# Optimization experiments

Hardware: AMD Instinct MI355X
Metric: run time of the kernel (lower is better)

Reference implementation:

```python
import jax, jax.numpy as jnp
import numpy as np

B, T, D = 256, 512, 32   # batch, seq_len, var_length (== input_size == output_size)
H, L = 256, 2            # hidden_size, num_layers


def setup_inputs() -> dict:
    key = jax.random.key(0)
    ks = jax.random.split(key, 16)
    s = 1.0 / np.sqrt(H)  # PyTorch LSTM/Linear default init range
    def u(k, shape):
        return jax.random.uniform(k, shape, jnp.float32, -s, s)
    inp = {"input": jax.random.normal(ks[0], (B, T, D), jnp.float32)}
    # encoder LSTM (b = b_ih + b_hh folded together); gate order i,f,g,o
    inp["enc_Wih0"] = u(ks[1], (4 * H, D)); inp["enc_Whh0"] = u(ks[2], (4 * H, H)); inp["enc_b0"] = u(ks[3], (4 * H,))
    inp["enc_Wih1"] = u(ks[4], (4 * H, H)); inp["enc_Whh1"] = u(ks[5], (4 * H, H)); inp["enc_b1"] = u(ks[6], (4 * H,))
    # decoder LSTM
    inp["dec_Wih0"] = u(ks[7], (4 * H, D)); inp["dec_Whh0"] = u(ks[8], (4 * H, H)); inp["dec_b0"] = u(ks[9], (4 * H,))
    inp["dec_Wih1"] = u(ks[10], (4 * H, H)); inp["dec_Whh1"] = u(ks[11], (4 * H, H)); inp["dec_b1"] = u(ks[12], (4 * H,))
    # output projection
    inp["fc_W"] = u(ks[13], (D, H)); inp["fc_b"] = u(ks[14], (D,))
    return inp


def _lstm_cell(x, h, c, Wih, Whh, b):
    g = x @ Wih.T + h @ Whh.T + b            # [B, 4H]
    i, f, gg, o = jnp.split(g, 4, axis=-1)   # PyTorch gate order i,f,g,o
    c = jax.nn.sigmoid(f) * c + jax.nn.sigmoid(i) * jnp.tanh(gg)
    h = jax.nn.sigmoid(o) * jnp.tanh(c)
    return h, c


def reference(input, enc_Wih0, enc_Whh0, enc_b0, enc_Wih1, enc_Whh1, enc_b1,
              dec_Wih0, dec_Whh0, dec_b0, dec_Wih1, dec_Whh1, dec_b1, fc_W, fc_b):
    b, t, d = input.shape
    hdim = enc_Whh0.shape[1]
    x = jnp.transpose(input, (1, 0, 2))  # time-major [T, B, D]

    # ----- encoder: 2-layer LSTM, keep final (h, c) per layer -----
    enc = [(enc_Wih0, enc_Whh0, enc_b0), (enc_Wih1, enc_Whh1, enc_b1)]
    hs, cs = [], []
    seq = x
    for Wih, Whh, bb in enc:
        def step(carry, xt, Wih=Wih, Whh=Whh, bb=bb):
            h, c = carry
            h, c = _lstm_cell(xt, h, c, Wih, Whh, bb)
            return (h, c), h
        z = jnp.zeros((b, hdim), input.dtype)
        (hT, cT), seq = jax.lax.scan(step, (z, z), seq)
        hs.append(hT); cs.append(cT)
    h0 = jnp.stack(hs)  # [L, B, H]
    c0 = jnp.stack(cs)

    dec = [(dec_Wih0, dec_Whh0, dec_b0), (dec_Wih1, dec_Whh1, dec_b1)]

    def dec_step(carry, _):
        xt, h, c = carry
        inp_l = xt
        new_h, new_c = [], []
        for l, (Wih, Whh, bb) in enumerate(dec):
            hl, cl = _lstm_cell(inp_l, h[l], c[l], Wih, Whh, bb)
            new_h.append(hl); new_c.append(cl)
            inp_l = hl
        pred = inp_l @ fc_W.T + fc_b  # [B, D]
        return (pred, jnp.stack(new_h), jnp.stack(new_c)), pred

    x0 = jnp.zeros((b, d), input.dtype)
    _, preds = jax.lax.scan(dec_step, (x0, h0, c0), None, length=t)  # [T, B, D]
    # cat along time then reverse (inv_idx)
    out = jnp.transpose(preds, (1, 0, 2))[:, ::-1, :]
    return out
```

## Files before the change

kernel.cpp:

```cpp
#include <hip/hip_runtime.h>

typedef __attribute__((ext_vector_type(8))) short bf16x8;
typedef __attribute__((ext_vector_type(4))) float f32x4;

#define MFMA16(a,b,c) __builtin_amdgcn_mfma_f32_16x16x32_bf16((a),(b),(c),0,0,0)


#define SZ_HBUF   (2*256*256*2)
#define OFF_H0H   0
#define OFF_H0L   (OFF_H0H + SZ_HBUF)
#define OFF_H1H   (OFF_H0L + SZ_HBUF)
#define OFF_H1L   (OFF_H1H + SZ_HBUF)
#define OFF_CFIN  (OFF_H1L + SZ_HBUF)
#define OFF_EW0H  (OFF_CFIN + 524288)
#define OFF_EW0L  (OFF_EW0H + 589824)
#define OFF_EW1H  (OFF_EW0L + 589824)
#define OFF_EW1L  (OFF_EW1H + 1048576)
#define OFF_DW0H  (OFF_EW1L + 1048576)
#define OFF_DW0L  (OFF_DW0H + 1048576)
#define OFF_DW1H  (OFF_DW0L + 1048576)
#define OFF_DW1L  (OFF_DW1H + 1048576)
#define OFF_BEFF  (OFF_DW1L + 1048576)
#define OFF_FCWH  (OFF_BEFF + 4096)
#define OFF_FCWL  (OFF_FCWH + 16384)
#define OFF_EFLG  (OFF_FCWL + 16384)
#define OFF_DFLG  (OFF_EFLG + 4096)

static __device__ __forceinline__ unsigned short f2bf(float f) {
  unsigned u = __float_as_uint(f);
  u = u + 0x7fffu + ((u >> 16) & 1u);
  return (unsigned short)(u >> 16);
}
static __device__ __forceinline__ float bf2f(unsigned short s) {
  return __uint_as_float(((unsigned)s) << 16);
}
static __device__ __forceinline__ float sigf(float x) {
  return 1.f / (1.f + __expf(-x));
}
static __device__ __forceinline__ float tanhsafe(float x) {
  float a = fabsf(x);
  float e = __expf(-2.f * a);
  float t = (1.f - e) / (1.f + e);
  return x < 0.f ? -t : t;
}
static __device__ __forceinline__ void st_hpair(float h, unsigned short* ph, unsigned short* pl) {
  unsigned short hi = f2bf(h);
  unsigned short lo = f2bf(h - bf2f(hi));
  __hip_atomic_store(ph, hi, __ATOMIC_RELAXED, __HIP_MEMORY_SCOPE_AGENT);
  __hip_atomic_store(pl, lo, __ATOMIC_RELAXED, __HIP_MEMORY_SCOPE_AGENT);
}
static __device__ __forceinline__ f32x4 ld16(const void* p) {
  f32x4 d;
  asm volatile("global_load_dwordx4 %0, %1, off sc0 sc1" : "=&v"(d) : "v"(p) : "memory");
  return d;
}
static __device__ __forceinline__ void wait_vm0() {
  asm volatile("s_waitcnt vmcnt(0)" ::: "memory");
  __builtin_amdgcn_sched_barrier(0);
}
static __device__ __forceinline__ void flag_barrier(unsigned* flags, int gc, unsigned round) {
  __syncthreads();
  if (threadIdx.x == 0)
    __hip_atomic_store(flags + gc, round, __ATOMIC_RELAXED, __HIP_MEMORY_SCOPE_AGENT);
  if (threadIdx.x < 64) {
    int l = threadIdx.x;
    for (;;) {
      unsigned v = (l < 16) ? __hip_atomic_load(flags + l, __ATOMIC_RELAXED, __HIP_MEMORY_SCOPE_AGENT)
                            : round;
      if (__all((int)(v >= round))) break;
    }
  }
  __syncthreads();
}

#define LDSF(base, row, kk) \
  (*(const bf16x8*)((base) + ((((row) << 9) | (lrow << 4) | ((kk) << 6)) ^ (((row) & 7) << 4))))

__global__ void k_prep_cat(int nrows, const float* __restrict__ s0, int K0,
                           const float* __restrict__ s1, int K1,
                           unsigned short* __restrict__ whi, unsigned short* __restrict__ wlo) {
  int K = K0 + K1;
  int tot = nrows * K;
  for (int idx = blockIdx.x * blockDim.x + threadIdx.x; idx < tot; idx += gridDim.x * blockDim.x) {
    int n = idx / K, k = idx - n * K;
    float v = (k < K0) ? s0[n * K0 + k] : s1[n * K1 + (k - K0)];
    unsigned short hi = f2bf(v);
    unsigned short lo = f2bf(v - bf2f(hi));
    whi[idx] = hi; wlo[idx] = lo;
  }
}
__global__ void k_prep_dec0(const float* __restrict__ Wih0, const float* __restrict__ Whh0,
                            const float* __restrict__ fcW,
                            unsigned short* __restrict__ whi, unsigned short* __restrict__ wlo) {
  int tot = 1024 * 512;
  for (int idx = blockIdx.x * blockDim.x + threadIdx.x; idx < tot; idx += gridDim.x * blockDim.x) {
    int n = idx >> 9, k = idx & 511;
    float v;
    if (k < 256) {
      v = 0.f;
      #pragma unroll
      for (int d = 0; d < 32; ++d) v += Wih0[n * 32 + d] * fcW[d * 256 + k];
    } else {
      v = Whh0[n * 256 + (k - 256)];
    }
    unsigned short hi = f2bf(v);
    unsigned short lo = f2bf(v - bf2f(hi));
    whi[idx] = hi; wlo[idx] = lo;
  }
}
__global__ void k_prep_beff(const float* __restrict__ Wih0, const float* __restrict__ b0,
                            const float* __restrict__ fcb, float* __restrict__ beff) {
  int n = blockIdx.x * blockDim.x + threadIdx.x;
  if (n < 1024) {
    float v = b0[n];
    #pragma unroll
    for (int d = 0; d < 32; ++d) v += Wih0[n * 32 + d] * fcb[d];
    beff[n] = v;
  }
}

__global__ __launch_bounds__(256, 1)
void k_encoder(const float* __restrict__ input,
               const unsigned short* __restrict__ w0hi, const unsigned short* __restrict__ w0lo,
               const unsigned short* __restrict__ w1hi, const unsigned short* __restrict__ w1lo,
               const float* __restrict__ b0, const float* __restrict__ b1,
               unsigned short* h0h, unsigned short* h0l,
               unsigned short* h1h, unsigned short* h1l,
               float* __restrict__ cfin, unsigned* flags)
{
  const int wg = blockIdx.x;
  const int gb = wg & 15, gc = wg >> 4;
  const int tid = threadIdx.x;
  const int wid = tid >> 6, lane = tid & 63;
  const int lcol = lane & 15, lrow = lane >> 4;
  const int r0 = gb * 16, u0 = gc * 16;
  const int wrow = wid * 256 + u0 + lcol;

  __shared__ char s_h0[2][8192];
  __shared__ char s_h1[2][8192];
  __shared__ float gA[4][16][17];
  __shared__ float gB[4][16][17];
  __shared__ float cb[2][16][16];

  cb[0][tid >> 4][tid & 15] = 0.f;
  cb[1][tid >> 4][tid & 15] = 0.f;

  const int srow = (tid >> 5) & 7;
  const int scol8 = (tid & 31) << 3;
  const int dA = ((srow << 9) | ((tid & 31) << 4)) ^ (srow << 4);
  const int dB = dA + 4096;

  bf16x8 w0h_[9], w0l_[9], w1h_[16], w1l_[16];
  {
    const unsigned short* p = w0hi + (size_t)wrow * 288 + lrow * 8;
    const unsigned short* q = w0lo + (size_t)wrow * 288 + lrow * 8;
    #pragma unroll
    for (int kk = 0; kk < 9; ++kk) {
      w0h_[kk] = *(const bf16x8*)(p + kk * 32);
      w0l_[kk] = *(const bf16x8*)(q + kk * 32);
    }
    const unsigned short* p1 = w1hi + (size_t)wrow * 512 + lrow * 8;
    const unsigned short* q1 = w1lo + (size_t)wrow * 512 + lrow * 8;
    #pragma unroll
    for (int kk = 0; kk < 16; ++kk) {
      w1h_[kk] = *(const bf16x8*)(p1 + kk * 32);
      w1l_[kk] = *(const bf16x8*)(q1 + kk * 32);
    }
  }
  const float bias0 = b0[wrow];
  const float bias1 = b1[wrow];
  unsigned* gflags = flags + gb * 64;
  __syncthreads();

  for (int k = 0; k <= 512; ++k) {
    const int rp = (k - 1) & 1;
    const int wp = k & 1;

    f32x4 ahh = {0.f,0.f,0.f,0.f}, ahl = {0.f,0.f,0.f,0.f}, alh = {0.f,0.f,0.f,0.f};
    union { bf16x8 v; unsigned short s[8]; } xh, xl;
    if (k < 512) {
      const float* px = input + (size_t)(r0 + lcol) * 16384 + (size_t)k * 32 + lrow * 8;
      f32x4 a = *(const f32x4*)px;
      f32x4 b = *(const f32x4*)(px + 4);
      #pragma unroll
      for (int j = 0; j < 4; ++j) {
        unsigned short t1 = f2bf(a[j]); xh.s[j] = t1;     xl.s[j]     = f2bf(a[j] - bf2f(t1));
        unsigned short t2 = f2bf(b[j]); xh.s[4 + j] = t2; xl.s[4 + j] = f2bf(b[j] - bf2f(t2));
      }
    }

    const unsigned short* p0h = h0h + (size_t)rp * 65536 + (size_t)(r0 + srow) * 256 + scol8;
    const unsigned short* p0l = h0l + (size_t)rp * 65536 + (size_t)(r0 + srow) * 256 + scol8;
    const unsigned short* p1h = h1h + (size_t)wp * 65536 + (size_t)(r0 + srow) * 256 + scol8;
    const unsigned short* p1l = h1l + (size_t)wp * 65536 + (size_t)(r0 + srow) * 256 + scol8;
    f32x4 v0 = ld16(p0h), v1 = ld16(p0h + 2048);
    f32x4 v2 = ld16(p0l), v3 = ld16(p0l + 2048);
    f32x4 v4 = ld16(p1h), v5 = ld16(p1h + 2048);
    f32x4 v6 = ld16(p1l), v7 = ld16(p1l + 2048);

    if (k < 512) {
      ahh = MFMA16(xh.v, w0h_[0], ahh);
      ahl = MFMA16(xh.v, w0l_[0], ahl);
      alh = MFMA16(xl.v, w0h_[0], alh);
    }

    wait_vm0();
    *(f32x4*)(s_h0[0] + dA) = v0; *(f32x4*)(s_h0[0] + dB) = v1;
    *(f32x4*)(s_h0[1] + dA) = v2; *(f32x4*)(s_h0[1] + dB) = v3;
    *(f32x4*)(s_h1[0] + dA) = v4; *(f32x4*)(s_h1[0] + dB) = v5;
    *(f32x4*)(s_h1[1] + dA) = v6; *(f32x4*)(s_h1[1] + dB) = v7;
    __syncthreads();

    bf16x8 f0h[8], f0l[8];
    #pragma unroll
    for (int kk = 0; kk < 8; ++kk) {
      f0h[kk] = LDSF(s_h0[0], lcol, kk);
      f0l[kk] = LDSF(s_h0[1], lcol, kk);
    }

    if (k < 512) {
      #pragma unroll
      for (int kk = 0; kk < 8; ++kk) {
        ahh = MFMA16(f0h[kk], w0h_[kk + 1], ahh);
        ahl = MFMA16(f0h[kk], w0l_[kk + 1], ahl);
        alh = MFMA16(f0l[kk], w0h_[kk + 1], alh);
      }
      f32x4 g = ahh + ahl + alh;
      #pragma unroll
      for (int r = 0; r < 4; ++r) gA[wid][lrow * 4 + r][lcol] = g[r] + bias0;
    }
    if (k >= 1) {
      f32x4 bhh = {0.f,0.f,0.f,0.f}, bhl = {0.f,0.f,0.f,0.f}, blh = {0.f,0.f,0.f,0.f};
      #pragma unroll
      for (int kk = 0; kk < 8; ++kk) {
        bhh = MFMA16(f0h[kk], w1h_[kk], bhh);
        bhl = MFMA16(f0h[kk], w1l_[kk], bhl);
        blh = MFMA16(f0l[kk], w1h_[kk], blh);
      }
      #pragma unroll
      for (int kk = 0; kk < 8; ++kk) {
        bf16x8 fh_ = LDSF(s_h1[0], lcol, kk);
        bf16x8 fl_ = LDSF(s_h1[1], lcol, kk);
        bhh = MFMA16(fh_, w1h_[kk + 8], bhh);
        bhl = MFMA16(fh_, w1l_[kk + 8], bhl);
        blh = MFMA16(fl_, w1h_[kk + 8], blh);
      }
      f32x4 g = bhh + bhl + blh;
      #pragma unroll
      for (int r = 0; r < 4; ++r) gB[wid][lrow * 4 + r][lcol] = g[r] + bias1;
    }
    __syncthreads();

    const int urow = tid >> 4, uu = tid & 15;
    if (k < 512) {
      float gi = gA[0][urow][uu], gf = gA[1][urow][uu];
      float gg = gA[2][urow][uu], go = gA[3][urow][uu];
      float c = sigf(gf) * cb[0][urow][uu] + sigf(gi) * tanhsafe(gg);
      cb[0][urow][uu] = c;
      float h = sigf(go) * tanhsafe(c);
      size_t off = (size_t)wp * 65536 + (size_t)(r0 + urow) * 256 + (u0 + uu);
      st_hpair(h, h0h + off, h0l + off);
    }
    if (k >= 1) {
      float gi = gB[0][urow][uu], gf = gB[1][urow][uu];
      float gg = gB[2][urow][uu], go = gB[3][urow][uu];
      float c = sigf(gf) * cb[1][urow][uu] + sigf(gi) * tanhsafe(gg);
      cb[1][urow][uu] = c;
      float h = sigf(go) * tanhsafe(c);
      size_t off = (size_t)rp * 65536 + (size_t)(r0 + urow) * 256 + (u0 + uu);
      st_hpair(h, h1h + off, h1l + off);
    }
    flag_barrier(gflags, gc, (unsigned)(k + 1));
  }

  const int urow = tid >> 4, uu = tid & 15;
  cfin[(size_t)(r0 + urow) * 256 + (u0 + uu)] = cb[0][urow][uu];
  cfin[65536 + (size_t)(r0 + urow) * 256 + (u0 + uu)] = cb[1][urow][uu];
}

__global__ __launch_bounds__(256, 1)
void k_decoder(const unsigned short* __restrict__ w0hi, const unsigned short* __restrict__ w0lo,
               const unsigned short* __restrict__ w1hi, const unsigned short* __restrict__ w1lo,
               const float* __restrict__ beff, const float* __restrict__ db0,
               const float* __restrict__ b1, const float* __restrict__ fcb,
               const unsigned short* __restrict__ fcwh_g, const unsigned short* __restrict__ fcwl_g,
               unsigned short* h0h, unsigned short* h0l,
               unsigned short* h1h, unsigned short* h1l,
               const float* __restrict__ cfin, float* __restrict__ out, unsigned* flags)
{
  const int wg = blockIdx.x;
  const int gb = wg & 15, gc = wg >> 4;
  const int tid = threadIdx.x;
  const int wid = tid >> 6, lane = tid & 63;
  const int lcol = lane & 15, lrow = lane >> 4;
  const int r0 = gb * 16, u0 = gc * 16;
  const int wrow = wid * 256 + u0 + lcol;

  __shared__ char s_h1[2][8192];
  __shared__ char s_h0[2][2][8192];
  __shared__ char s_fcw[2][16384];
  __shared__ float gA[4][16][17];
  __shared__ float cb[2][16][16];

  const int srow = (tid >> 5) & 7;
  const int scol8 = (tid & 31) << 3;
  const int dA = ((srow << 9) | ((tid & 31) << 4)) ^ (srow << 4);
  const int dB = dA + 4096;

  {
    const int urow = tid >> 4, uu = tid & 15;
    cb[0][urow][uu] = cfin[(size_t)(r0 + urow) * 256 + (u0 + uu)];
    cb[1][urow][uu] = cfin[65536 + (size_t)(r0 + urow) * 256 + (u0 + uu)];
  }
  {
    const unsigned short* q1h = h1h + 65536 + (size_t)(r0 + srow) * 256 + scol8;
    const unsigned short* q1l = h1l + 65536 + (size_t)(r0 + srow) * 256 + scol8;
    const unsigned short* q0h = h0h + 65536 + (size_t)(r0 + srow) * 256 + scol8;
    const unsigned short* q0l = h0l + 65536 + (size_t)(r0 + srow) * 256 + scol8;
    f32x4 v0 = ld16(q1h), v1 = ld16(q1h + 2048);
    f32x4 v2 = ld16(q1l), v3 = ld16(q1l + 2048);
    f32x4 v4 = ld16(q0h), v5 = ld16(q0h + 2048);
    f32x4 v6 = ld16(q0l), v7 = ld16(q0l + 2048);
    f32x4 fh0 = ld16(fcwh_g + (size_t)srow * 256 + scol8);
    f32x4 fh1 = ld16(fcwh_g + (size_t)(srow + 8) * 256 + scol8);
    f32x4 fh2 = ld16(fcwh_g + (size_t)(srow + 16) * 256 + scol8);
    f32x4 fh3 = ld16(fcwh_g + (size_t)(srow + 24) * 256 + scol8);
    f32x4 fl0 = ld16(fcwl_g + (size_t)srow * 256 + scol8);
    f32x4 fl1 = ld16(fcwl_g + (size_t)(srow + 8) * 256 + scol8);
    f32x4 fl2 = ld16(fcwl_g + (size_t)(srow + 16) * 256 + scol8);
    f32x4 fl3 = ld16(fcwl_g + (size_t)(srow + 24) * 256 + scol8);
    wait_vm0();
    *(f32x4*)(s_h1[0] + dA) = v0;    *(f32x4*)(s_h1[0] + dB) = v1;
    *(f32x4*)(s_h1[1] + dA) = v2;    *(f32x4*)(s_h1[1] + dB) = v3;
    *(f32x4*)(s_h0[1][0] + dA) = v4; *(f32x4*)(s_h0[1][0] + dB) = v5;
    *(f32x4*)(s_h0[1][1] + dA) = v6; *(f32x4*)(s_h0[1][1] + dB) = v7;
    *(f32x4*)(s_fcw[0] + dA) = fh0;          *(f32x4*)(s_fcw[0] + dA + 4096) = fh1;
    *(f32x4*)(s_fcw[0] + dA + 8192) = fh2;   *(f32x4*)(s_fcw[0] + dA + 12288) = fh3;
    *(f32x4*)(s_fcw[1] + dA) = fl0;          *(f32x4*)(s_fcw[1] + dA + 4096) = fl1;
    *(f32x4*)(s_fcw[1] + dA + 8192) = fl2;   *(f32x4*)(s_fcw[1] + dA + 12288) = fl3;
  }

  bf16x8 w0h_[16], w0l_[16], w1h_[16], w1l_[16];
  {
    const unsigned short* p = w0hi + (size_t)wrow * 512 + lrow * 8;
    const unsigned short* q = w0lo + (size_t)wrow * 512 + lrow * 8;
    #pragma unroll
    for (int kk = 0; kk < 16; ++kk) {
      w0h_[kk] = *(const bf16x8*)(p + kk * 32);
      w0l_[kk] = *(const bf16x8*)(q + kk * 32);
    }
    const unsigned short* p1 = w1hi + (size_t)wrow * 512 + lrow * 8;
    const unsigned short* q1 = w1lo + (size_t)wrow * 512 + lrow * 8;
    #pragma unroll
    for (int kk = 0; kk < 16; ++kk) {
      w1h_[kk] = *(const bf16x8*)(p1 + kk * 32);
      w1l_[kk] = *(const bf16x8*)(q1 + kk * 32);
    }
  }
  const float bias0 = beff[wrow], bias0t0 = db0[wrow], bias1 = b1[wrow];
  const float fcbv = (wid < 2) ? fcb[wid * 16 + lcol] : 0.f;
  unsigned* gflags = flags + gb * 64;
  __syncthreads();

  bf16x8 h1h_r[8], h1l_r[8];

  for (int t = 0; t < 512; ++t) {
    const int wp = t & 1, rp = 1 - wp;

    f32x4 a0, a1, a2, a3;
    if (t > 0) {
      const unsigned short* ph = h1h + (size_t)rp * 65536 + (size_t)(r0 + srow) * 256 + scol8;
      const unsigned short* pl = h1l + (size_t)rp * 65536 + (size_t)(r0 + srow) * 256 + scol8;
      a0 = ld16(ph); a1 = ld16(ph + 2048);
      a2 = ld16(pl); a3 = ld16(pl + 2048);
    }
    f32x4 ahh = {0.f,0.f,0.f,0.f}, ahl = {0.f,0.f,0.f,0.f}, alh = {0.f,0.f,0.f,0.f};
    #pragma unroll
    for (int kk = 0; kk < 8; ++kk) {
      bf16x8 fh_ = LDSF(s_h0[rp][0], lcol, kk);
      bf16x8 fl_ = LDSF(s_h0[rp][1], lcol, kk);
      ahh = MFMA16(fh_, w0h_[kk + 8], ahh);
      ahl = MFMA16(fh_, w0l_[kk + 8], ahl);
      alh = MFMA16(fl_, w0h_[kk + 8], alh);
    }
    if (t > 0) {
      wait_vm0();
      *(f32x4*)(s_h1[0] + dA) = a0; *(f32x4*)(s_h1[0] + dB) = a1;
      *(f32x4*)(s_h1[1] + dA) = a2; *(f32x4*)(s_h1[1] + dB) = a3;
    }
    __syncthreads();
    #pragma unroll
    for (int kk = 0; kk < 8; ++kk) {
      h1h_r[kk] = LDSF(s_h1[0], lcol, kk);
      h1l_r[kk] = LDSF(s_h1[1], lcol, kk);
    }
    if (t > 0) {
      #pragma unroll
      for (int kk = 0; kk < 8; ++kk) {
        ahh = MFMA16(h1h_r[kk], w0h_[kk], ahh);
        ahl = MFMA16(h1h_r[kk], w0l_[kk], ahl);
        alh = MFMA16(h1l_r[kk], w0h_[kk], alh);
      }
    }
    {
      f32x4 g = ahh + ahl + alh;
      float bb = (t == 0) ? bias0t0 : bias0;
      #pragma unroll
      for (int r = 0; r < 4; ++r) gA[wid][lrow * 4 + r][lcol] = g[r] + bb;
    }
    __syncthreads();
    {
      const int urow = tid >> 4, uu = tid & 15;
      float gi = gA[0][urow][uu], gf = gA[1][urow][uu];
      float gg = gA[2][urow][uu], go = gA[3][urow][uu];
      float c = sigf(gf) * cb[0][urow][uu] + sigf(gi) * tanhsafe(gg);
      cb[0][urow][uu] = c;
      float h = sigf(go) * tanhsafe(c);
      size_t off = (size_t)wp * 65536 + (size_t)(r0 + urow) * 256 + (u0 + uu);
      st_hpair(h, h0h + off, h0l + off);
    }
    flag_barrier(gflags, gc, (unsigned)(2 * t + 1));

    f32x4 b0v, b1v, b2v, b3v;
    {
      const unsigned short* ph = h0h + (size_t)wp * 65536 + (size_t)(r0 + srow) * 256 + scol8;
      const unsigned short* pl = h0l + (size_t)wp * 65536 + (size_t)(r0 + srow) * 256 + scol8;
      b0v = ld16(ph); b1v = ld16(ph + 2048);
      b2v = ld16(pl); b3v = ld16(pl + 2048);
    }
    f32x4 bhh = {0.f,0.f,0.f,0.f}, bhl = {0.f,0.f,0.f,0.f}, blh = {0.f,0.f,0.f,0.f};
    #pragma unroll
    for (int kk = 0; kk < 8; ++kk) {
      bhh = MFMA16(h1h_r[kk], w1h_[kk + 8], bhh);
      bhl = MFMA16(h1h_r[kk], w1l_[kk + 8], bhl);
      blh = MFMA16(h1l_r[kk], w1h_[kk + 8], blh);
    }
    f32x4 p0 = {0.f,0.f,0.f,0.f}, p1 = {0.f,0.f,0.f,0.f}, p2 = {0.f,0.f,0.f,0.f};
    if (t > 0 && wid < 2) {
      #pragma unroll
      for (int kk = 0; kk < 8; ++kk) {
        bf16x8 fh_ = LDSF(s_fcw[0], wid * 16 + lcol, kk);
        bf16x8 fl_ = LDSF(s_fcw[1], wid * 16 + lcol, kk);
        p0 = MFMA16(h1h_r[kk], fh_, p0);
        p1 = MFMA16(h1h_r[kk], fl_, p1);
        p2 = MFMA16(h1l_r[kk], fh_, p2);
      }
    }
    wait_vm0();
    if (t > 0 && wid < 2 && gc == 0) {
      #pragma unroll
      for (int j = 0; j < 4; ++j)
        out[(size_t)(r0 + lrow * 4 + j) * 16384 + (size_t)(512 - t) * 32 + wid * 16 + lcol] =
            p0[j] + p1[j] + p2[j] + fcbv;
    }
    *(f32x4*)(s_h0[wp][0] + dA) = b0v; *(f32x4*)(s_h0[wp][0] + dB) = b1v;
    *(f32x4*)(s_h0[wp][1] + dA) = b2v; *(f32x4*)(s_h0[wp][1] + dB) = b3v;
    __syncthreads();
    {
      #pragma unroll
      for (int kk = 0; kk < 8; ++kk) {
        bf16x8 fh_ = LDSF(s_h0[wp][0], lcol, kk);
        bf16x8 fl_ = LDSF(s_h0[wp][1], lcol, kk);
        bhh = MFMA16(fh_, w1h_[kk], bhh);
        bhl = MFMA16(fh_, w1l_[kk], bhl);
        blh = MFMA16(fl_, w1h_[kk], blh);
      }
      f32x4 g = bhh + bhl + blh;
      #pragma unroll
      for (int r = 0; r < 4; ++r) gA[wid][lrow * 4 + r][lcol] = g[r] + bias1;
    }
    __syncthreads();
    {
      const int urow = tid >> 4, uu = tid & 15;
      float gi = gA[0][urow][uu], gf = gA[1][urow][uu];
      float gg = gA[2][urow][uu], go = gA[3][urow][uu];
      float c = sigf(gf) * cb[1][urow][uu] + sigf(gi) * tanhsafe(gg);
      cb[1][urow][uu] = c;
      float h = sigf(go) * tanhsafe(c);
      size_t off = (size_t)wp * 65536 + (size_t)(r0 + urow) * 256 + (u0 + uu);
      st_hpair(h, h1h + off, h1l + off);
    }
    flag_barrier(gflags, gc, (unsigned)(2 * t + 2));
  }

  {
    const unsigned short* ph = h1h + 65536 + (size_t)(r0 + srow) * 256 + scol8;
    const unsigned short* pl = h1l + 65536 + (size_t)(r0 + srow) * 256 + scol8;
    f32x4 v0 = ld16(ph), v1 = ld16(ph + 2048);
    f32x4 v2 = ld16(pl), v3 = ld16(pl + 2048);
    wait_vm0();
    *(f32x4*)(s_h1[0] + dA) = v0; *(f32x4*)(s_h1[0] + dB) = v1;
    *(f32x4*)(s_h1[1] + dA) = v2; *(f32x4*)(s_h1[1] + dB) = v3;
  }
  __syncthreads();
  if (wid < 2) {
    f32x4 p0 = {0.f,0.f,0.f,0.f}, p1 = {0.f,0.f,0.f,0.f}, p2 = {0.f,0.f,0.f,0.f};
    #pragma unroll
    for (int kk = 0; kk < 8; ++kk) {
      bf16x8 ah = LDSF(s_h1[0], lcol, kk);
      bf16x8 al = LDSF(s_h1[1], lcol, kk);
      bf16x8 fh_ = LDSF(s_fcw[0], wid * 16 + lcol, kk);
      bf16x8 fl_ = LDSF(s_fcw[1], wid * 16 + lcol, kk);
      p0 = MFMA16(ah, fh_, p0);
      p1 = MFMA16(ah, fl_, p1);
      p2 = MFMA16(al, fh_, p2);
    }
    if (gc == 0) {
      #pragma unroll
      for (int j = 0; j < 4; ++j)
        out[(size_t)(r0 + lrow * 4 + j) * 16384 + wid * 16 + lcol] = p0[j] + p1[j] + p2[j] + fcbv;
    }
  }
}

extern "C" void kernel_launch(void* const* d_in, const int* in_sizes, int n_in,
                              void* d_out, int out_size, void* d_ws, size_t ws_size,
                              hipStream_t stream) {
  (void)in_sizes; (void)n_in; (void)ws_size;
  const float* input = (const float*)d_in[0];
  const float* eWih0 = (const float*)d_in[1];
  const float* eWhh0 = (const float*)d_in[2];
  const float* eb0   = (const float*)d_in[3];
  const float* eWih1 = (const float*)d_in[4];
  const float* eWhh1 = (const float*)d_in[5];
  const float* eb1   = (const float*)d_in[6];
  const float* dWih0 = (const float*)d_in[7];
  const float* dWhh0 = (const float*)d_in[8];
  const float* db0   = (const float*)d_in[9];
  const float* dWih1 = (const float*)d_in[10];
  const float* dWhh1 = (const float*)d_in[11];
  const float* db1   = (const float*)d_in[12];
  const float* fcW   = (const float*)d_in[13];
  const float* fcb   = (const float*)d_in[14];

  char* ws = (char*)d_ws;
  unsigned short* h0h = (unsigned short*)(ws + OFF_H0H);
  unsigned short* h0l = (unsigned short*)(ws + OFF_H0L);
  unsigned short* h1h = (unsigned short*)(ws + OFF_H1H);
  unsigned short* h1l = (unsigned short*)(ws + OFF_H1L);
  float* cfin = (float*)(ws + OFF_CFIN);
  unsigned short* ew0h = (unsigned short*)(ws + OFF_EW0H);
  unsigned short* ew0l = (unsigned short*)(ws + OFF_EW0L);
  unsigned short* ew1h = (unsigned short*)(ws + OFF_EW1H);
  unsigned short* ew1l = (unsigned short*)(ws + OFF_EW1L);
  unsigned short* dw0h = (unsigned short*)(ws + OFF_DW0H);
  unsigned short* dw0l = (unsigned short*)(ws + OFF_DW0L);
  unsigned short* dw1h = (unsigned short*)(ws + OFF_DW1H);
  unsigned short* dw1l = (unsigned short*)(ws + OFF_DW1L);
  float* beff = (float*)(ws + OFF_BEFF);
  unsigned short* fcwh = (unsigned short*)(ws + OFF_FCWH);
  unsigned short* fcwl = (unsigned short*)(ws + OFF_FCWL);
  unsigned* eflg = (unsigned*)(ws + OFF_EFLG);
  unsigned* dflg = (unsigned*)(ws + OFF_DFLG);

  hipMemsetAsync(d_out, 0, (size_t)out_size * sizeof(float), stream);
  hipMemsetAsync(ws + OFF_H0H, 0, (size_t)4 * SZ_HBUF, stream);
  hipMemsetAsync(ws + OFF_EFLG, 0, 8192, stream);

  k_prep_cat<<<1024, 256, 0, stream>>>(1024, eWih0, 32,  eWhh0, 256, ew0h, ew0l);
  k_prep_cat<<<1024, 256, 0, stream>>>(1024, eWih1, 256, eWhh1, 256, ew1h, ew1l);
  k_prep_cat<<<1024, 256, 0, stream>>>(1024, dWih1, 256, dWhh1, 256, dw1h, dw1l);
  k_prep_cat<<<64, 256, 0, stream>>>(32, fcW, 256, fcW, 0, fcwh, fcwl);
  k_prep_dec0<<<1024, 256, 0, stream>>>(dWih0, dWhh0, fcW, dw0h, dw0l);
  k_prep_beff<<<4, 256, 0, stream>>>(dWih0, db0, fcb, beff);

  k_encoder<<<256, 256, 0, stream>>>(input, ew0h, ew0l, ew1h, ew1l, eb0, eb1,
                                     h0h, h0l, h1h, h1l, cfin, eflg);
  k_decoder<<<256, 256, 0, stream>>>(dw0h, dw0l, dw1h, dw1l, beff, db0, db1, fcb,
                                     fcwh, fcwl, h0h, h0l, h1h, h1l, cfin,
                                     (float*)d_out, dflg);
}
```

Baseline: 4.125 ms.

## Replace flag barriers with tagged hidden-state words polled by consumers

Removes the per-step global flag barrier in both encoder and decoder. Each hidden value is now packed as hi/lo bf16 in one 32-bit word whose low two bits carry a rotating step tag, and consumers spin re-loading only the chunks whose tags are stale. Cell state moves from LDS to registers, and the next input timestep is prefetched one step ahead. This cuts barrier round trips and halves the number of h stores, at the cost of dropping two mantissa bits of the low bf16 part and relying on a mod-3 tag to keep buffers from aliasing across steps.

```diff
diff --git a/kernel.cpp b/kernel.cpp
--- a/kernel.cpp
+++ b/kernel.cpp
@@ -2,16 +2,14 @@
 
 typedef __attribute__((ext_vector_type(8))) short bf16x8;
 typedef __attribute__((ext_vector_type(4))) float f32x4;
+typedef __attribute__((ext_vector_type(4))) unsigned u32x4;
 
 #define MFMA16(a,b,c) __builtin_amdgcn_mfma_f32_16x16x32_bf16((a),(b),(c),0,0,0)
 
 
-#define SZ_HBUF   (2*256*256*2)
-#define OFF_H0H   0
-#define OFF_H0L   (OFF_H0H + SZ_HBUF)
-#define OFF_H1H   (OFF_H0L + SZ_HBUF)
-#define OFF_H1L   (OFF_H1H + SZ_HBUF)
-#define OFF_CFIN  (OFF_H1L + SZ_HBUF)
+#define OFF_H0    0
+#define OFF_H1    (OFF_H0 + 524288)
+#define OFF_CFIN  (OFF_H1 + 524288)
 #define OFF_EW0H  (OFF_CFIN + 524288)
 #define OFF_EW0L  (OFF_EW0H + 589824)
 #define OFF_EW1H  (OFF_EW0L + 589824)
@@ -23,8 +21,6 @@
 #define OFF_BEFF  (OFF_DW1L + 1048576)
 #define OFF_FCWH  (OFF_BEFF + 4096)
 #define OFF_FCWL  (OFF_FCWH + 16384)
-#define OFF_EFLG  (OFF_FCWL + 16384)
-#define OFF_DFLG  (OFF_EFLG + 4096)
 
 static __device__ __forceinline__ unsigned short f2bf(float f) {
   unsigned u = __float_as_uint(f);
@@ -43,11 +39,16 @@
   float t = (1.f - e) / (1.f + e);
   return x < 0.f ? -t : t;
 }
-static __device__ __forceinline__ void st_hpair(float h, unsigned short* ph, unsigned short* pl) {
+static __device__ __forceinline__ void st_htag(unsigned* dst, float h, unsigned tag) {
   unsigned short hi = f2bf(h);
   unsigned short lo = f2bf(h - bf2f(hi));
-  __hip_atomic_store(ph, hi, __ATOMIC_RELAXED, __HIP_MEMORY_SCOPE_AGENT);
-  __hip_atomic_store(pl, lo, __ATOMIC_RELAXED, __HIP_MEMORY_SCOPE_AGENT);
+  unsigned w = ((unsigned)hi << 16) | ((unsigned)lo & 0xFFFCu) | tag;
+  __hip_atomic_store(dst, w, __ATOMIC_RELAXED, __HIP_MEMORY_SCOPE_AGENT);
+}
+static __device__ __forceinline__ u32x4 ld16u(const void* p) {
+  u32x4 d;
+  asm volatile("global_load_dwordx4 %0, %1, off sc0 sc1" : "=&v"(d) : "v"(p) : "memory");
+  return d;
 }
 static __device__ __forceinline__ f32x4 ld16(const void* p) {
   f32x4 d;
@@ -58,19 +59,53 @@
   asm volatile("s_waitcnt vmcnt(0)" ::: "memory");
   __builtin_amdgcn_sched_barrier(0);
 }
-static __device__ __forceinline__ void flag_barrier(unsigned* flags, int gc, unsigned round) {
-  __syncthreads();
-  if (threadIdx.x == 0)
-    __hip_atomic_store(flags + gc, round, __ATOMIC_RELAXED, __HIP_MEMORY_SCOPE_AGENT);
-  if (threadIdx.x < 64) {
-    int l = threadIdx.x;
-    for (;;) {
-      unsigned v = (l < 16) ? __hip_atomic_load(flags + l, __ATOMIC_RELAXED, __HIP_MEMORY_SCOPE_AGENT)
-                            : round;
-      if (__all((int)(v >= round))) break;
-    }
-  }
-  __syncthreads();
+static __device__ __forceinline__ int tagok(u32x4 c, unsigned tag) {
+  return ((c[0] & 3u) == tag) & ((c[1] & 3u) == tag) & ((c[2] & 3u) == tag) & ((c[3] & 3u) == tag);
+}
+static __device__ __forceinline__ void stg_issue(u32x4* c, const unsigned* p) {
+  c[0] = ld16u(p); c[1] = ld16u(p + 4); c[2] = ld16u(p + 8); c[3] = ld16u(p + 12);
+}
+static __device__ __forceinline__ void stg_validate(u32x4* c, const unsigned* p, unsigned tag) {
+  for (;;) {
+    int o0 = tagok(c[0], tag), o1 = tagok(c[1], tag), o2 = tagok(c[2], tag), o3 = tagok(c[3], tag);
+    if (o0 & o1 & o2 & o3) break;
+    if (!o0) c[0] = ld16u(p);
+    if (!o1) c[1] = ld16u(p + 4);
+    if (!o2) c[2] = ld16u(p + 8);
+    if (!o3) c[3] = ld16u(p + 12);
+    wait_vm0();
+  }
+}
+static __device__ __forceinline__ void stg_validate2(u32x4* a, const unsigned* pa, unsigned ta,
+                                                     u32x4* b, const unsigned* pb, unsigned tb) {
+  for (;;) {
+    int a0 = tagok(a[0], ta), a1 = tagok(a[1], ta), a2 = tagok(a[2], ta), a3 = tagok(a[3], ta);
+    int b0 = tagok(b[0], tb), b1 = tagok(b[1], tb), b2 = tagok(b[2], tb), b3 = tagok(b[3], tb);
+    if (a0 & a1 & a2 & a3 & b0 & b1 & b2 & b3) break;
+    if (!a0) a[0] = ld16u(pa);     if (!a1) a[1] = ld16u(pa + 4);
+    if (!a2) a[2] = ld16u(pa + 8); if (!a3) a[3] = ld16u(pa + 12);
+    if (!b0) b[0] = ld16u(pb);     if (!b1) b[1] = ld16u(pb + 4);
+    if (!b2) b[2] = ld16u(pb + 8); if (!b3) b[3] = ld16u(pb + 12);
+    wait_vm0();
+  }
+}
+static __device__ __forceinline__ unsigned hp2(unsigned a, unsigned b) { return (a >> 16) | (b & 0xFFFF0000u); }
+static __device__ __forceinline__ unsigned lp2(unsigned a, unsigned b) { return (a & 0xFFFFu) | (b << 16); }
+static __device__ __forceinline__ void stg_unpack(const u32x4* c, char* ldsH, char* ldsL, int row, int ucol) {
+  u32x4 hA, hB, lA, lB;
+  hA[0] = hp2(c[0][0], c[0][1]); hA[1] = hp2(c[0][2], c[0][3]);
+  hA[2] = hp2(c[1][0], c[1][1]); hA[3] = hp2(c[1][2], c[1][3]);
+  hB[0] = hp2(c[2][0], c[2][1]); hB[1] = hp2(c[2][2], c[2][3]);
+  hB[2] = hp2(c[3][0], c[3][1]); hB[3] = hp2(c[3][2], c[3][3]);
+  lA[0] = lp2(c[0][0], c[0][1]); lA[1] = lp2(c[0][2], c[0][3]);
+  lA[2] = lp2(c[1][0], c[1][1]); lA[3] = lp2(c[1][2], c[1][3]);
+  lB[0] = lp2(c[2][0], c[2][1]); lB[1] = lp2(c[2][2], c[2][3]);
+  lB[2] = lp2(c[3][0], c[3][1]); lB[3] = lp2(c[3][2], c[3][3]);
+  int sw = (row & 7) << 4;
+  int a0 = ((row << 9) | (ucol << 5)) ^ sw;
+  int a1 = ((row << 9) | (ucol << 5) | 16) ^ sw;
+  *(u32x4*)(ldsH + a0) = hA; *(u32x4*)(ldsH + a1) = hB;
+  *(u32x4*)(ldsL + a0) = lA; *(u32x4*)(ldsL + a1) = lB;
 }
 
 #define LDSF(base, row, kk) \
@@ -124,9 +159,7 @@
                const unsigned short* __restrict__ w0hi, const unsigned short* __restrict__ w0lo,
                const unsigned short* __restrict__ w1hi, const unsigned short* __restrict__ w1lo,
                const float* __restrict__ b0, const float* __restrict__ b1,
-               unsigned short* h0h, unsigned short* h0l,
-               unsigned short* h1h, unsigned short* h1l,
-               float* __restrict__ cfin, unsigned* flags)
+               unsigned* h0, unsigned* h1, float* __restrict__ cfin)
 {
   const int wg = blockIdx.x;
   const int gb = wg & 15, gc = wg >> 4;
@@ -135,20 +168,13 @@
   const int lcol = lane & 15, lrow = lane >> 4;
   const int r0 = gb * 16, u0 = gc * 16;
   const int wrow = wid * 256 + u0 + lcol;
+  const int row = tid >> 4, ucol = tid & 15;
+  const int urow = tid >> 4, uu = tid & 15;
 
   __shared__ char s_h0[2][8192];
   __shared__ char s_h1[2][8192];
   __shared__ float gA[4][16][17];
   __shared__ float gB[4][16][17];
-  __shared__ float cb[2][16][16];
-
-  cb[0][tid >> 4][tid & 15] = 0.f;
-  cb[1][tid >> 4][tid & 15] = 0.f;
-
-  const int srow = (tid >> 5) & 7;
-  const int scol8 = (tid & 31) << 3;
-  const int dA = ((srow << 9) | ((tid & 31) << 4)) ^ (srow << 4);
-  const int dB = dA + 4096;
 
   bf16x8 w0h_[9], w0l_[9], w1h_[16], w1l_[16];
   {
@@ -169,35 +195,43 @@
   }
   const float bias0 = b0[wrow];
   const float bias1 = b1[wrow];
-  unsigned* gflags = flags + gb * 64;
+  float c0reg = 0.f, c1reg = 0.f;
+
+  const float* pxrow = input + (size_t)(r0 + lcol) * 16384 + lrow * 8;
+  union { bf16x8 v; unsigned short s[8]; } xh, xl;
+  {
+    f32x4 a = *(const f32x4*)(pxrow);
+    f32x4 b = *(const f32x4*)(pxrow + 4);
+    #pragma unroll
+    for (int j = 0; j < 4; ++j) {
+      unsigned short t1 = f2bf(a[j]); xh.s[j] = t1;     xl.s[j]     = f2bf(a[j] - bf2f(t1));
+      unsigned short t2 = f2bf(b[j]); xh.s[4 + j] = t2; xl.s[4 + j] = f2bf(b[j] - bf2f(t2));
+    }
+  }
+  const unsigned* g0base = h0 + (size_t)(r0 + row) * 256 + ucol * 16;
+  const unsigned* g1base = h1 + (size_t)(r0 + row) * 256 + ucol * 16;
+  unsigned* s0base = h0 + (size_t)(r0 + urow) * 256 + (u0 + uu);
+  unsigned* s1base = h1 + (size_t)(r0 + urow) * 256 + (u0 + uu);
   __syncthreads();
 
   for (int k = 0; k <= 512; ++k) {
     const int rp = (k - 1) & 1;
     const int wp = k & 1;
+    const unsigned e0 = (k == 0) ? 0u : (unsigned)(1 + ((k - 1) % 3));
+    const unsigned e1 = (k < 2) ? 0u : (unsigned)(1 + ((k - 2) % 3));
+
+    const unsigned* p0 = g0base + (size_t)rp * 65536;
+    const unsigned* p1 = g1base + (size_t)wp * 65536;
+    u32x4 c0[4], c1[4];
+    stg_issue(c0, p0);
+    stg_issue(c1, p1);
+    f32x4 nxa, nxb;
+    if (k < 511) {
+      nxa = ld16(pxrow + (size_t)(k + 1) * 32);
+      nxb = ld16(pxrow + (size_t)(k + 1) * 32 + 4);
+    }
 
     f32x4 ahh = {0.f,0.f,0.f,0.f}, ahl = {0.f,0.f,0.f,0.f}, alh = {0.f,0.f,0.f,0.f};
-    union { bf16x8 v; unsigned short s[8]; } xh, xl;
-    if (k < 512) {
-      const float* px = input + (size_t)(r0 + lcol) * 16384 + (size_t)k * 32 + lrow * 8;
-      f32x4 a = *(const f32x4*)px;
-      f32x4 b = *(const f32x4*)(px + 4);
-      #pragma unroll
-      for (int j = 0; j < 4; ++j) {
-        unsigned short t1 = f2bf(a[j]); xh.s[j] = t1;     xl.s[j]     = f2bf(a[j] - bf2f(t1));
-        unsigned short t2 = f2bf(b[j]); xh.s[4 + j] = t2; xl.s[4 + j] = f2bf(b[j] - bf2f(t2));
-      }
-    }
-
-    const unsigned short* p0h = h0h + (size_t)rp * 65536 + (size_t)(r0 + srow) * 256 + scol8;
-    const unsigned short* p0l = h0l + (size_t)rp * 65536 + (size_t)(r0 + srow) * 256 + scol8;
-    const unsigned short* p1h = h1h + (size_t)wp * 65536 + (size_t)(r0 + srow) * 256 + scol8;
-    const unsigned short* p1l = h1l + (size_t)wp * 65536 + (size_t)(r0 + srow) * 256 + scol8;
-    f32x4 v0 = ld16(p0h), v1 = ld16(p0h + 2048);
-    f32x4 v2 = ld16(p0l), v3 = ld16(p0l + 2048);
-    f32x4 v4 = ld16(p1h), v5 = ld16(p1h + 2048);
-    f32x4 v6 = ld16(p1l), v7 = ld16(p1l + 2048);
-
     if (k < 512) {
       ahh = MFMA16(xh.v, w0h_[0], ahh);
       ahl = MFMA16(xh.v, w0l_[0], ahl);
@@ -205,10 +239,16 @@
     }
 
     wait_vm0();
-    *(f32x4*)(s_h0[0] + dA) = v0; *(f32x4*)(s_h0[0] + dB) = v1;
-    *(f32x4*)(s_h0[1] + dA) = v2; *(f32x4*)(s_h0[1] + dB) = v3;
-    *(f32x4*)(s_h1[0] + dA) = v4; *(f32x4*)(s_h1[0] + dB) = v5;
-    *(f32x4*)(s_h1[1] + dA) = v6; *(f32x4*)(s_h1[1] + dB) = v7;
+    stg_validate2(c0, p0, e0, c1, p1, e1);
+    stg_unpack(c0, s_h0[0], s_h0[1], row, ucol);
+    stg_unpack(c1, s_h1[0], s_h1[1], row, ucol);
+    if (k < 511) {
+      #pragma unroll
+      for (int j = 0; j < 4; ++j) {
+        unsigned short t1 = f2bf(nxa[j]); xh.s[j] = t1;     xl.s[j]     = f2bf(nxa[j] - bf2f(t1));
+        unsigned short t2 = f2bf(nxb[j]); xh.s[4 + j] = t2; xl.s[4 + j] = f2bf(nxb[j] - bf2f(t2));
+      }
+    }
     __syncthreads();
 
     bf16x8 f0h[8], f0l[8];
@@ -251,31 +291,26 @@
     }
     __syncthreads();
 
-    const int urow = tid >> 4, uu = tid & 15;
     if (k < 512) {
       float gi = gA[0][urow][uu], gf = gA[1][urow][uu];
       float gg = gA[2][urow][uu], go = gA[3][urow][uu];
-      float c = sigf(gf) * cb[0][urow][uu] + sigf(gi) * tanhsafe(gg);
-      cb[0][urow][uu] = c;
+      float c = sigf(gf) * c0reg + sigf(gi) * tanhsafe(gg);
+      c0reg = c;
       float h = sigf(go) * tanhsafe(c);
-      size_t off = (size_t)wp * 65536 + (size_t)(r0 + urow) * 256 + (u0 + uu);
-      st_hpair(h, h0h + off, h0l + off);
+      st_htag(s0base + (size_t)wp * 65536, h, (unsigned)(1 + (k % 3)));
     }
     if (k >= 1) {
       float gi = gB[0][urow][uu], gf = gB[1][urow][uu];
       float gg = gB[2][urow][uu], go = gB[3][urow][uu];
-      float c = sigf(gf) * cb[1][urow][uu] + sigf(gi) * tanhsafe(gg);
-      cb[1][urow][uu] = c;
+      float c = sigf(gf) * c1reg + sigf(gi) * tanhsafe(gg);
+      c1reg = c;
       float h = sigf(go) * tanhsafe(c);
-      size_t off = (size_t)rp * 65536 + (size_t)(r0 + urow) * 256 + (u0 + uu);
-      st_hpair(h, h1h + off, h1l + off);
-    }
-    flag_barrier(gflags, gc, (unsigned)(k + 1));
-  }
-
-  const int urow = tid >> 4, uu = tid & 15;
-  cfin[(size_t)(r0 + urow) * 256 + (u0 + uu)] = cb[0][urow][uu];
-  cfin[65536 + (size_t)(r0 + urow) * 256 + (u0 + uu)] = cb[1][urow][uu];
+      st_htag(s1base + (size_t)rp * 65536, h, (unsigned)(1 + ((k - 1) % 3)));
+    }
+  }
+
+  cfin[(size_t)(r0 + urow) * 256 + (u0 + uu)] = c0reg;
+  cfin[65536 + (size_t)(r0 + urow) * 256 + (u0 + uu)] = c1reg;
 }
 
 __global__ __launch_bounds__(256, 1)
@@ -284,9 +319,8 @@
                const float* __restrict__ beff, const float* __restrict__ db0,
                const float* __restrict__ b1, const float* __restrict__ fcb,
                const unsigned short* __restrict__ fcwh_g, const unsigned short* __restrict__ fcwl_g,
-               unsigned short* h0h, unsigned short* h0l,
-               unsigned short* h1h, unsigned short* h1l,
-               const float* __restrict__ cfin, float* __restrict__ out, unsigned* flags)
+               unsigned* h0, unsigned* h1,
+               const float* __restrict__ cfin, float* __restrict__ out)
 {
   const int wg = blockIdx.x;
   const int gb = wg & 15, gc = wg >> 4;
@@ -295,32 +329,29 @@
   const int lcol = lane & 15, lrow = lane >> 4;
   const int r0 = gb * 16, u0 = gc * 16;
   const int wrow = wid * 256 + u0 + lcol;
+  const int row = tid >> 4, ucol = tid & 15;
+  const int urow = tid >> 4, uu = tid & 15;
 
   __shared__ char s_h1[2][8192];
   __shared__ char s_h0[2][2][8192];
   __shared__ char s_fcw[2][16384];
   __shared__ float gA[4][16][17];
-  __shared__ float cb[2][16][16];
-
-  const int srow = (tid >> 5) & 7;
-  const int scol8 = (tid & 31) << 3;
-  const int dA = ((srow << 9) | ((tid & 31) << 4)) ^ (srow << 4);
-  const int dB = dA + 4096;
+
+  float c0reg = cfin[(size_t)(r0 + urow) * 256 + (u0 + uu)];
+  float c1reg = cfin[65536 + (size_t)(r0 + urow) * 256 + (u0 + uu)];
+
+  const unsigned* g0base = h0 + (size_t)(r0 + row) * 256 + ucol * 16;
+  const unsigned* g1base = h1 + (size_t)(r0 + row) * 256 + ucol * 16;
+  unsigned* s0base = h0 + (size_t)(r0 + urow) * 256 + (u0 + uu);
+  unsigned* s1base = h1 + (size_t)(r0 + urow) * 256 + (u0 + uu);
 
   {
-    const int urow = tid >> 4, uu = tid & 15;
-    cb[0][urow][uu] = cfin[(size_t)(r0 + urow) * 256 + (u0 + uu)];
-    cb[1][urow][uu] = cfin[65536 + (size_t)(r0 + urow) * 256 + (u0 + uu)];
-  }
-  {
-    const unsigned short* q1h = h1h + 65536 + (size_t)(r0 + srow) * 256 + scol8;
-    const unsigned short* q1l = h1l + 65536 + (size_t)(r0 + srow) * 256 + scol8;
-    const unsigned short* q0h = h0h + 65536 + (size_t)(r0 + srow) * 256 + scol8;
-    const unsigned short* q0l = h0l + 65536 + (size_t)(r0 + srow) * 256 + scol8;
-    f32x4 v0 = ld16(q1h), v1 = ld16(q1h + 2048);
-    f32x4 v2 = ld16(q1l), v3 = ld16(q1l + 2048);
-    f32x4 v4 = ld16(q0h), v5 = ld16(q0h + 2048);
-    f32x4 v6 = ld16(q0l), v7 = ld16(q0l + 2048);
+    const int srow = (tid >> 5) & 7;
+    const int scol8 = (tid & 31) << 3;
+    const int dA = ((srow << 9) | ((tid & 31) << 4)) ^ (srow << 4);
+    u32x4 ch1[4], ch0[4];
+    stg_issue(ch1, g1base + 65536);
+    stg_issue(ch0, g0base + 65536);
     f32x4 fh0 = ld16(fcwh_g + (size_t)srow * 256 + scol8);
     f32x4 fh1 = ld16(fcwh_g + (size_t)(srow + 8) * 256 + scol8);
     f32x4 fh2 = ld16(fcwh_g + (size_t)(srow + 16) * 256 + scol8);
@@ -330,10 +361,8 @@
     f32x4 fl2 = ld16(fcwl_g + (size_t)(srow + 16) * 256 + scol8);
     f32x4 fl3 = ld16(fcwl_g + (size_t)(srow + 24) * 256 + scol8);
     wait_vm0();
-    *(f32x4*)(s_h1[0] + dA) = v0;    *(f32x4*)(s_h1[0] + dB) = v1;
-    *(f32x4*)(s_h1[1] + dA) = v2;    *(f32x4*)(s_h1[1] + dB) = v3;
-    *(f32x4*)(s_h0[1][0] + dA) = v4; *(f32x4*)(s_h0[1][0] + dB) = v5;
-    *(f32x4*)(s_h0[1][1] + dA) = v6; *(f32x4*)(s_h0[1][1] + dB) = v7;
+    stg_unpack(ch1, s_h1[0], s_h1[1], row, ucol);
+    stg_unpack(ch0, s_h0[1][0], s_h0[1][1], row, ucol);
     *(f32x4*)(s_fcw[0] + dA) = fh0;          *(f32x4*)(s_fcw[0] + dA + 4096) = fh1;
     *(f32x4*)(s_fcw[0] + dA + 8192) = fh2;   *(f32x4*)(s_fcw[0] + dA + 12288) = fh3;
     *(f32x4*)(s_fcw[1] + dA) = fl0;          *(f32x4*)(s_fcw[1] + dA + 4096) = fl1;
@@ -359,21 +388,19 @@
   }
   const float bias0 = beff[wrow], bias0t0 = db0[wrow], bias1 = b1[wrow];
   const float fcbv = (wid < 2) ? fcb[wid * 16 + lcol] : 0.f;
-  unsigned* gflags = flags + gb * 64;
   __syncthreads();
 
   bf16x8 h1h_r[8], h1l_r[8];
 
   for (int t = 0; t < 512; ++t) {
     const int wp = t & 1, rp = 1 - wp;
-
-    f32x4 a0, a1, a2, a3;
-    if (t > 0) {
-      const unsigned short* ph = h1h + (size_t)rp * 65536 + (size_t)(r0 + srow) * 256 + scol8;
-      const unsigned short* pl = h1l + (size_t)rp * 65536 + (size_t)(r0 + srow) * 256 + scol8;
-      a0 = ld16(ph); a1 = ld16(ph + 2048);
-      a2 = ld16(pl); a3 = ld16(pl + 2048);
-    }
+    const unsigned tag0 = (unsigned)(1 + ((t + 1) % 3));
+    const unsigned tag1 = (unsigned)(1 + ((t + 2) % 3));
+    const unsigned tag1p = (unsigned)(1 + ((t + 1) % 3));
+
+    u32x4 ch[4];
+    const unsigned* pA = g1base + (size_t)rp * 65536;
+    if (t > 0) stg_issue(ch, pA);
     f32x4 ahh = {0.f,0.f,0.f,0.f}, ahl = {0.f,0.f,0.f,0.f}, alh = {0.f,0.f,0.f,0.f};
     #pragma unroll
     for (int kk = 0; kk < 8; ++kk) {
@@ -385,8 +412,8 @@
     }
     if (t > 0) {
       wait_vm0();
-      *(f32x4*)(s_h1[0] + dA) = a0; *(f32x4*)(s_h1[0] + dB) = a1;
-      *(f32x4*)(s_h1[1] + dA) = a2; *(f32x4*)(s_h1[1] + dB) = a3;
+      stg_validate(ch, pA, tag1p);
+      stg_unpack(ch, s_h1[0], s_h1[1], row, ucol);
     }
     __syncthreads();
     #pragma unroll
@@ -410,24 +437,16 @@
     }
     __syncthreads();
     {
-      const int urow = tid >> 4, uu = tid & 15;
       float gi = gA[0][urow][uu], gf = gA[1][urow][uu];
       float gg = gA[2][urow][uu], go = gA[3][urow][uu];
-      float c = sigf(gf) * cb[0][urow][uu] + sigf(gi) * tanhsafe(gg);
-      cb[0][urow][uu] = c;
+      float c = sigf(gf) * c0reg + sigf(gi) * tanhsafe(gg);
+      c0reg = c;
       float h = sigf(go) * tanhsafe(c);
-      size_t off = (size_t)wp * 65536 + (size_t)(r0 + urow) * 256 + (u0 + uu);
-      st_hpair(h, h0h + off, h0l + off);
-    }
-    flag_barrier(gflags, gc, (unsigned)(2 * t + 1));
-
-    f32x4 b0v, b1v, b2v, b3v;
-    {
-      const unsigned short* ph = h0h + (size_t)wp * 65536 + (size_t)(r0 + srow) * 256 + scol8;
-      const unsigned short* pl = h0l + (size_t)wp * 65536 + (size_t)(r0 + srow) * 256 + scol8;
-      b0v = ld16(ph); b1v = ld16(ph + 2048);
-      b2v = ld16(pl); b3v = ld16(pl + 2048);
-    }
+      st_htag(s0base + (size_t)wp * 65536, h, tag0);
+    }
+
+    const unsigned* pB = g0base + (size_t)wp * 65536;
+    stg_issue(ch, pB);
     f32x4 bhh = {0.f,0.f,0.f,0.f}, bhl = {0.f,0.f,0.f,0.f}, blh = {0.f,0.f,0.f,0.f};
     #pragma unroll
     for (int kk = 0; kk < 8; ++kk) {
@@ -447,14 +466,14 @@
       }
     }
     wait_vm0();
+    stg_validate(ch, pB, tag0);
     if (t > 0 && wid < 2 && gc == 0) {
       #pragma unroll
       for (int j = 0; j < 4; ++j)
         out[(size_t)(r0 + lrow * 4 + j) * 16384 + (size_t)(512 - t) * 32 + wid * 16 + lcol] =
             p0[j] + p1[j] + p2[j] + fcbv;
     }
-    *(f32x4*)(s_h0[wp][0] + dA) = b0v; *(f32x4*)(s_h0[wp][0] + dB) = b1v;
-    *(f32x4*)(s_h0[wp][1] + dA) = b2v; *(f32x4*)(s_h0[wp][1] + dB) = b3v;
+    stg_unpack(ch, s_h0[wp][0], s_h0[wp][1], row, ucol);
     __syncthreads();
     {
       #pragma unroll
@@ -471,26 +490,22 @@
     }
     __syncthreads();
     {
-      const int urow = tid >> 4, uu = tid & 15;
       float gi = gA[0][urow][uu], gf = gA[1][urow][uu];
       float gg = gA[2][urow][uu], go = gA[3][urow][uu];
-      float c = sigf(gf) * cb[1][urow][uu] + sigf(gi) * tanhsafe(gg);
-      cb[1][urow][uu] = c;
+      float c = sigf(gf) * c1reg + sigf(gi) * tanhsafe(gg);
+      c1reg = c;
       float h = sigf(go) * tanhsafe(c);
-      size_t off = (size_t)wp * 65536 + (size_t)(r0 + urow) * 256 + (u0 + uu);
-      st_hpair(h, h1h + off, h1l + off);
-    }
-    flag_barrier(gflags, gc, (unsigned)(2 * t + 2));
+      st_htag(s1base + (size_t)wp * 65536, h, tag1);
+    }
   }
 
   {
-    const unsigned short* ph = h1h + 65536 + (size_t)(r0 + srow) * 256 + scol8;
-    const unsigned short* pl = h1l + 65536 + (size_t)(r0 + srow) * 256 + scol8;
-    f32x4 v0 = ld16(ph), v1 = ld16(ph + 2048);
-    f32x4 v2 = ld16(pl), v3 = ld16(pl + 2048);
+    u32x4 ch[4];
+    const unsigned* pT = g1base + 65536;
+    stg_issue(ch, pT);
     wait_vm0();
-    *(f32x4*)(s_h1[0] + dA) = v0; *(f32x4*)(s_h1[0] + dB) = v1;
-    *(f32x4*)(s_h1[1] + dA) = v2; *(f32x4*)(s_h1[1] + dB) = v3;
+    stg_validate(ch, pT, (unsigned)(1 + (513 % 3)));
+    stg_unpack(ch, s_h1[0], s_h1[1], row, ucol);
   }
   __syncthreads();
   if (wid < 2) {
@@ -534,10 +549,8 @@
   const float* fcb   = (const float*)d_in[14];
 
   char* ws = (char*)d_ws;
-  unsigned short* h0h = (unsigned short*)(ws + OFF_H0H);
-  unsigned short* h0l = (unsigned short*)(ws + OFF_H0L);
-  unsigned short* h1h = (unsigned short*)(ws + OFF_H1H);
-  unsigned short* h1l = (unsigned short*)(ws + OFF_H1L);
+  unsigned* h0 = (unsigned*)(ws + OFF_H0);
+  unsigned* h1 = (unsigned*)(ws + OFF_H1);
   float* cfin = (float*)(ws + OFF_CFIN);
   unsigned short* ew0h = (unsigned short*)(ws + OFF_EW0H);
   unsigned short* ew0l = (unsigned short*)(ws + OFF_EW0L);
@@ -550,12 +563,9 @@
   float* beff = (float*)(ws + OFF_BEFF);
   unsigned short* fcwh = (unsigned short*)(ws + OFF_FCWH);
   unsigned short* fcwl = (unsigned short*)(ws + OFF_FCWL);
-  unsigned* eflg = (unsigned*)(ws + OFF_EFLG);
-  unsigned* dflg = (unsigned*)(ws + OFF_DFLG);
 
   hipMemsetAsync(d_out, 0, (size_t)out_size * sizeof(float), stream);
-  hipMemsetAsync(ws + OFF_H0H, 0, (size_t)4 * SZ_HBUF, stream);
-  hipMemsetAsync(ws + OFF_EFLG, 0, 8192, stream);
+  hipMemsetAsync(ws + OFF_H0, 0, 2 * 524288, stream);
 
   k_prep_cat<<<1024, 256, 0, stream>>>(1024, eWih0, 32,  eWhh0, 256, ew0h, ew0l);
   k_prep_cat<<<1024, 256, 0, stream>>>(1024, eWih1, 256, eWhh1, 256, ew1h, ew1l);
@@ -565,8 +575,7 @@
   k_prep_beff<<<4, 256, 0, stream>>>(dWih0, db0, fcb, beff);
 
   k_encoder<<<256, 256, 0, stream>>>(input, ew0h, ew0l, ew1h, ew1l, eb0, eb1,
-                                     h0h, h0l, h1h, h1l, cfin, eflg);
+                                     h0, h1, cfin);
   k_decoder<<<256, 256, 0, stream>>>(dw0h, dw0l, dw1h, dw1l, beff, db0, db1, fcb,
-                                     fcwh, fcwl, h0h, h0l, h1h, h1l, cfin,
-                                     (float*)d_out, dflg);
-}
+                                     fcwh, fcwl, h0, h1, cfin, (float*)d_out);
+}
```

After: 6.400 ms. 1.55x slower.
